# Kernel optimization log

Measured on AMD Instinct MI355X. Metric: run time of the kernel, lower is better.

## Reference

```python
import jax, jax.numpy as jnp
import numpy as np

NV = 117000
NE = 468000
EMB = 300
IN_DIM = 768
BATCH = 4096
HID = 500
NUM_LABELS = 2


def setup_inputs() -> dict:
    key = jax.random.key(0)
    ks = jax.random.split(key, 12)
    inp = {
        "input_tensor": jax.random.normal(ks[0], (BATCH, IN_DIM), dtype=jnp.float32),
        "node": jax.random.randint(ks[1], (BATCH,), 0, NV, dtype=jnp.int64),
        "edge_row": jax.random.randint(ks[2], (NE,), 0, NV, dtype=jnp.int32),
        "edge_col": jax.random.randint(ks[3], (NE,), 0, NV, dtype=jnp.int32),
        # learned parameters
        "H0": jax.random.normal(ks[4], (NV, EMB), dtype=jnp.float32) * 1.0,
        "W1": jax.random.normal(ks[5], (EMB, EMB), dtype=jnp.float32) * 0.01,
        "W2": jax.random.normal(ks[6], (EMB, EMB), dtype=jnp.float32) * 0.01,
        "Wa": jax.random.normal(ks[7], (IN_DIM + EMB, HID), dtype=jnp.float32) * 0.03,
        "ba": jnp.zeros((HID,), dtype=jnp.float32),
        "Wb": jax.random.normal(ks[8], (HID, HID), dtype=jnp.float32) * 0.04,
        "bb": jnp.zeros((HID,), dtype=jnp.float32),
        "Wc": jax.random.normal(ks[9], (HID, NUM_LABELS), dtype=jnp.float32) * 0.04,
        "bc": jnp.zeros((NUM_LABELS,), dtype=jnp.float32),
    }
    return inp


def reference(input_tensor, node, edge_row, edge_col, H0, W1, W2, Wa, ba, Wb, bb, Wc, bc):
    nV = H0.shape[0]
    # symmetric normalization D^{-1/2} A D^{-1/2} from edge list (duplicates sum, as in csr)
    deg = jax.ops.segment_sum(jnp.ones_like(edge_row, dtype=H0.dtype), edge_row, num_segments=nV)
    dinv = jnp.where(deg > 0, deg ** -0.5, 0.0)
    vals = dinv[edge_row] * dinv[edge_col]  # [nE]

    def spmm(X):  # LM @ X via gather + segment_sum
        return jax.ops.segment_sum(vals[:, None] * X[edge_col], edge_row, num_segments=nV)

    H1 = jax.nn.sigmoid(spmm(H0 @ W1))        # [nV, EMB]
    H2 = jax.nn.sigmoid(spmm(H1 @ W2))        # [nV, EMB]
    fc = jnp.concatenate([H2[node], input_tensor], axis=1)  # [B, EMB+IN_DIM]
    h = jax.nn.sigmoid(fc @ Wa + ba)
    h = jax.nn.sigmoid(h @ Wb + bb)
    return h @ Wc + bc                        # [B, NUM_LABELS]
```

## Files before the change

### kernel.cpp

```cpp
#include <hip/hip_runtime.h>
#include <hip/hip_bf16.h>

typedef __hip_bfloat16 bf16;

#define NVX 117000
#define NEX 468000
#define EMB 300
#define STR 320
#define IN_DIM 768
#define BATCH 4096
#define HID 500
#define FCK 1088
#define HPAD 512
#define NB 458
#define NEB 1829

#define CAP1 32768
#define CAP2 4096

#define PRE_W12 (384*STR)
#define PRE_WA  (HPAD*FCK)
#define PRE_WB  (HPAD*HPAD)
#define PRE_TOT (2*PRE_W12 + PRE_WA + PRE_WB)
#define PRE_BLK ((PRE_TOT+255)/256)

typedef __attribute__((ext_vector_type(8))) short frag8;
typedef __attribute__((ext_vector_type(4))) float f32x4;

__device__ __forceinline__ float sigmoidf_(float x){ return 1.0f/(1.0f + __expf(-x)); }
__device__ __forceinline__ float bfs2f(short s){
  return __uint_as_float(((unsigned int)(unsigned short)s) << 16);
}
__device__ __forceinline__ short f2bfs(float f){
  bf16 b = __float2bfloat16(f);
  return *(short*)&b;
}

__device__ __forceinline__ void gload_lds16(const bf16* g, bf16* l){
  __builtin_amdgcn_global_load_lds((const __attribute__((address_space(1))) void*)g,
                                   (__attribute__((address_space(3))) void*)l, 16, 0, 0);
}


__global__ __launch_bounds__(256) void k_setup(const int* __restrict__ erow,
                                               const int* __restrict__ node,
                                               int* __restrict__ deg,
                                               int* __restrict__ flag2,
                                               const float* __restrict__ W1,
                                               const float* __restrict__ W2,
                                               const float* __restrict__ Wa,
                                               const float* __restrict__ Wb,
                                               bf16* __restrict__ Wt1,
                                               bf16* __restrict__ Wt2,
                                               bf16* __restrict__ Wat,
                                               bf16* __restrict__ Wbt){
  long i = (long)blockIdx.x*256 + threadIdx.x;
  if (i < NEX) atomicAdd(&deg[erow[i]], 1);
  if (i < BATCH) flag2[node[i]] = 1;

  if (i < 2*PRE_W12){
    const float* W = (i < PRE_W12) ? W1 : W2;
    bf16* o = (i < PRE_W12) ? Wt1 : Wt2;
    int j = (int)((i < PRE_W12) ? i : i - PRE_W12);
    int n = j / STR, k = j % STR;
    float v = (n < EMB && k < EMB) ? W[k*EMB + n] : 0.0f;
    o[j] = __float2bfloat16(v);
    return;
  }
  i -= 2*PRE_W12;
  if (i < PRE_WA){
    int n = (int)(i / FCK), k = (int)(i % FCK);
    float v = 0.0f;
    if (n < HID){
      if (k < EMB)        v = Wa[(size_t)k*HID + n];
      else if (k >= STR)  v = Wa[(size_t)(k-(STR-EMB))*HID + n];
    }
    Wat[i] = __float2bfloat16(v);
    return;
  }
  i -= PRE_WA;
  if (i < PRE_WB){
    int n = (int)(i / HPAD), k = (int)(i % HPAD);
    float v = (n < HID && k < HID) ? Wb[(size_t)k*HID + n] : 0.0f;
    Wbt[i] = __float2bfloat16(v);
  }
}


__global__ __launch_bounds__(256) void k_flag1ps(const int* __restrict__ erow,
                                                 const int* __restrict__ ecol,
                                                 const int* __restrict__ flag2,
                                                 const int* __restrict__ deg,
                                                 int* __restrict__ flag1,
                                                 float* __restrict__ dinv,
                                                 int* __restrict__ bsum){
  int t = threadIdx.x;
  long j = (long)blockIdx.x*256 + t;
  if (j < NEX && flag2[erow[j]]) flag1[ecol[j]] = 1;

  if (blockIdx.x < NB){
    __shared__ int s[256];
    int i = blockIdx.x*256 + t;
    int d = (i < NVX) ? deg[i] : 0;
    if (i < NVX) dinv[i] = d > 0 ? rsqrtf((float)d) : 0.0f;
    s[t] = d;
    __syncthreads();
    #pragma unroll
    for (int off=128; off; off>>=1){
      if (t < off) s[t] += s[t+off];
      __syncthreads();
    }
    if (t == 0) bsum[blockIdx.x] = s[0];
  }
}


__global__ __launch_bounds__(256) void k_writeptr2(const int* __restrict__ deg,
                                                   const int* __restrict__ bsum,
                                                   int* __restrict__ rowptr,
                                                   int* __restrict__ cursor){
  __shared__ int sb[256];
  __shared__ int s[256];
  int t = threadIdx.x;
  int b = blockIdx.x;
  int acc = 0;
  for (int j = t; j < b; j += 256) acc += bsum[j];
  sb[t] = acc;
  __syncthreads();
  #pragma unroll
  for (int off=128; off; off>>=1){
    if (t < off) sb[t] += sb[t+off];
    __syncthreads();
  }
  int boff = sb[0];

  int i = b*256 + t;
  int v = (i < NVX) ? deg[i] : 0;
  s[t] = v; __syncthreads();
  #pragma unroll
  for (int off=1; off<256; off<<=1){
    int u = (t>=off) ? s[t-off] : 0;
    __syncthreads();
    s[t] += u;
    __syncthreads();
  }
  if (i < NVX){
    int e = boff + s[t] - v;
    rowptr[i] = e;
    cursor[i] = e;
  }
  if (b == 0 && t == 0) rowptr[NVX] = NEX;
}


__global__ __launch_bounds__(256) void k_edgec(const int* __restrict__ erow,
                                               const int* __restrict__ ecol,
                                               const float* __restrict__ dinv,
                                               const int* __restrict__ flag1,
                                               const int* __restrict__ flag2,
                                               int* __restrict__ cursor,
                                               int* __restrict__ ccol,
                                               float* __restrict__ cval,
                                               int* __restrict__ L1, int* __restrict__ inv1,
                                               int* __restrict__ L2, int* __restrict__ inv2,
                                               int* __restrict__ counts){
  long j = (long)blockIdx.x*256 + threadIdx.x;
  if (j < NEX){
    int r = erow[j];
    if (flag1[r] | flag2[r]){
      int c = ecol[j];
      int p = atomicAdd(&cursor[r], 1);
      ccol[p] = c;
      cval[p] = dinv[r]*dinv[c];
    }
  }
  int v = (int)j;
  if (v < NVX){
    if (flag1[v]){ int idx = atomicAdd(&counts[0], 1); if (idx < CAP1){ L1[idx] = v; inv1[v] = idx; } }
    if (flag2[v]){ int idx = atomicAdd(&counts[1], 1); if (idx < CAP2){ L2[idx] = v; inv2[v] = idx; } }
  }
}


__global__ __launch_bounds__(256) void k_spmm1(const int* __restrict__ rowptr,
                                               const int* __restrict__ ccol,
                                               const float* __restrict__ cval,
                                               const float* __restrict__ H0,
                                               const int* __restrict__ L1,
                                               const int* __restrict__ counts,
                                               bf16* __restrict__ Gc1){
  int i = (int)((blockIdx.x*blockDim.x + threadIdx.x) >> 6);
  int lane = threadIdx.x & 63;
  if (lane >= 40) return;
  int n1 = counts[0]; if (n1 > CAP1) n1 = CAP1;
  int n1pad = (n1 + 127) & ~127;
  if (i >= n1pad) return;
  int c0 = lane*8;
  bool hv1 = (c0 + 3) < EMB;
  bool hv2 = (c0 + 7) < EMB;
  float acc[8] = {0.f,0.f,0.f,0.f,0.f,0.f,0.f,0.f};
  if (i < n1 && hv1){
    int v = L1[i];
    int e0 = rowptr[v], e1 = rowptr[v+1];
    int e = e0;
    for (; e + 1 < e1; e += 2){
      float va = cval[e], vb = cval[e+1];
      const float* xa = H0 + (size_t)ccol[e  ]*EMB + c0;
      const float* xb = H0 + (size_t)ccol[e+1]*EMB + c0;
      float4 a0 = *(const float4*)xa;
      float4 b0 = *(const float4*)xb;
      float4 a1 = hv2 ? *(const float4*)(xa+4) : make_float4(0,0,0,0);
      float4 b1 = hv2 ? *(const float4*)(xb+4) : make_float4(0,0,0,0);
      acc[0] += va*a0.x + vb*b0.x;  acc[1] += va*a0.y + vb*b0.y;
      acc[2] += va*a0.z + vb*b0.z;  acc[3] += va*a0.w + vb*b0.w;
      acc[4] += va*a1.x + vb*b1.x;  acc[5] += va*a1.y + vb*b1.y;
      acc[6] += va*a1.z + vb*b1.z;  acc[7] += va*a1.w + vb*b1.w;
    }
    if (e < e1){
      float va = cval[e];
      const float* xa = H0 + (size_t)ccol[e]*EMB + c0;
      float4 a0 = *(const float4*)xa;
      float4 a1 = hv2 ? *(const float4*)(xa+4) : make_float4(0,0,0,0);
      acc[0] += va*a0.x; acc[1] += va*a0.y; acc[2] += va*a0.z; acc[3] += va*a0.w;
      acc[4] += va*a1.x; acc[5] += va*a1.y; acc[6] += va*a1.z; acc[7] += va*a1.w;
    }
  }
  frag8 o;
  #pragma unroll
  for (int j=0;j<8;++j) o[j] = f2bfs(acc[j]);
  *(frag8*)(Gc1 + (size_t)i*STR + c0) = o;
}


__global__ __launch_bounds__(256) void k_spmm2(const int* __restrict__ rowptr,
                                               const int* __restrict__ ccol,
                                               const float* __restrict__ cval,
                                               const bf16* __restrict__ Hc1,
                                               const int* __restrict__ inv1,
                                               const int* __restrict__ L2,
                                               const int* __restrict__ counts,
                                               bf16* __restrict__ Gc2){
  int i = (int)((blockIdx.x*blockDim.x + threadIdx.x) >> 6);
  int lane = threadIdx.x & 63;
  if (lane >= 40) return;
  int n2 = counts[1]; if (n2 > CAP2) n2 = CAP2;
  int n2pad = (n2 + 127) & ~127;
  if (i >= n2pad) return;
  float acc[8] = {0.f,0.f,0.f,0.f,0.f,0.f,0.f,0.f};
  if (i < n2){
    int v = L2[i];
    int e0 = rowptr[v], e1 = rowptr[v+1];
    int e = e0;
    for (; e + 1 < e1; e += 2){
      float va = cval[e], vb = cval[e+1];
      frag8 xa = *(const frag8*)(Hc1 + (size_t)inv1[ccol[e  ]]*STR + lane*8);
      frag8 xb = *(const frag8*)(Hc1 + (size_t)inv1[ccol[e+1]]*STR + lane*8);
      #pragma unroll
      for (int j=0;j<8;++j) acc[j] += va*bfs2f(xa[j]) + vb*bfs2f(xb[j]);
    }
    if (e < e1){
      float va = cval[e];
      frag8 xa = *(const frag8*)(Hc1 + (size_t)inv1[ccol[e]]*STR + lane*8);
      #pragma unroll
      for (int j=0;j<8;++j) acc[j] += va*bfs2f(xa[j]);
    }
  }
  frag8 o;
  #pragma unroll
  for (int j=0;j<8;++j) o[j] = f2bfs(acc[j]);
  *(frag8*)(Gc2 + (size_t)i*STR + lane*8) = o;
}


__global__ __launch_bounds__(256) void k_gemm_node(const bf16* __restrict__ A,
                                                   const bf16* __restrict__ Wt,
                                                   bf16* __restrict__ C,
                                                   const int* __restrict__ counts, int which){
  const int row0 = blockIdx.y * 128;
  if (row0 >= counts[which]) return;
  __shared__ bf16 As[128*32];
  __shared__ bf16 Bs[128*32];
  const int tid  = threadIdx.x;
  const int wv   = tid >> 6;
  const int lane = tid & 63;
  const int n0   = blockIdx.x * 128;
  const int wm = wv & 1, wn = wv >> 1;
  const int srow = lane >> 2;
  const int schk = lane & 3;
  const int fr = lane & 15, fq = lane >> 4;

  f32x4 acc[4][4];
  #pragma unroll
  for (int i=0;i<4;++i)
    #pragma unroll
    for (int j=0;j<4;++j) acc[i][j] = (f32x4)(0.0f);

  for (int k0 = 0; k0 < STR; k0 += 32){
    const bf16* ag = A + (size_t)(row0 + wv*16 + srow)*STR + k0 + schk*8;
    gload_lds16(ag,           As + wv*512 + lane*8);
    gload_lds16(ag + 64*STR,  As + 2048 + wv*512 + lane*8);
    const bf16* bg = Wt + (size_t)(n0 + wv*16 + srow)*STR + k0 + schk*8;
    gload_lds16(bg,           Bs + wv*512 + lane*8);
    gload_lds16(bg + 64*STR,  Bs + 2048 + wv*512 + lane*8);
    __syncthreads();
    frag8 a[4], b[4];
    #pragma unroll
    for (int mi=0;mi<4;++mi)
      a[mi] = *(const frag8*)(As + (wm*64 + mi*16 + fr)*32 + fq*8);
    #pragma unroll
    for (int ni=0;ni<4;++ni)
      b[ni] = *(const frag8*)(Bs + (wn*64 + ni*16 + fr)*32 + fq*8);
    #pragma unroll
    for (int mi=0;mi<4;++mi)
      #pragma unroll
      for (int ni=0;ni<4;++ni)
        acc[mi][ni] = __builtin_amdgcn_mfma_f32_16x16x32_bf16(a[mi], b[ni], acc[mi][ni], 0, 0, 0);
    __syncthreads();
  }

  #pragma unroll
  for (int mi=0;mi<4;++mi){
    int row = row0 + wm*64 + mi*16 + fq*4;
    #pragma unroll
    for (int ni=0;ni<4;++ni){
      int col = n0 + wn*64 + ni*16 + fr;
      if (col < STR){
        bf16* cp = C + (size_t)row*STR + col;
        #pragma unroll
        for (int r=0;r<4;++r){
          float v = (col < EMB) ? sigmoidf_(acc[mi][ni][r]) : 0.0f;
          cp[(size_t)r*STR] = __float2bfloat16(v);
        }
      }
    }
  }
}


__global__ __launch_bounds__(256) void k_fc1g(const bf16* __restrict__ Hc2,
                                              const int* __restrict__ node,
                                              const int* __restrict__ inv2,
                                              const float* __restrict__ input,
                                              const bf16* __restrict__ Wat,
                                              const float* __restrict__ ba,
                                              bf16* __restrict__ h1){
  __shared__ bf16 As[128*32];
  __shared__ bf16 Bs[128*32];
  const int tid  = threadIdx.x;
  const int wv   = tid >> 6;
  const int lane = tid & 63;
  const int row0 = blockIdx.y * 128;
  const int n0   = blockIdx.x * 128;
  const int wm = wv & 1, wn = wv >> 1;
  const int srow = lane >> 2;
  const int schk = lane & 3;
  const int fr = lane & 15, fq = lane >> 4;

  const int nlo = inv2[node[row0 + wv*16 + srow]];
  const int nhi = inv2[node[row0 + 64 + wv*16 + srow]];

  f32x4 acc[4][4];
  #pragma unroll
  for (int i=0;i<4;++i)
    #pragma unroll
    for (int j=0;j<4;++j) acc[i][j] = (f32x4)(0.0f);

  for (int k0 = 0; k0 < FCK; k0 += 32){
    if (k0 < STR){
      gload_lds16(Hc2 + (size_t)nlo*STR + k0 + schk*8, As + wv*512 + lane*8);
      gload_lds16(Hc2 + (size_t)nhi*STR + k0 + schk*8, As + 2048 + wv*512 + lane*8);
    } else {
      int c = k0 - STR + schk*8;
      int m0 = wv*16 + srow;
      float4 u0 = *(const float4*)(input + (size_t)(row0+m0)*IN_DIM + c);
      float4 u1 = *(const float4*)(input + (size_t)(row0+m0)*IN_DIM + c + 4);
      frag8 t0;
      t0[0]=f2bfs(u0.x); t0[1]=f2bfs(u0.y); t0[2]=f2bfs(u0.z); t0[3]=f2bfs(u0.w);
      t0[4]=f2bfs(u1.x); t0[5]=f2bfs(u1.y); t0[6]=f2bfs(u1.z); t0[7]=f2bfs(u1.w);
      *(frag8*)(As + m0*32 + schk*8) = t0;
      int m1 = 64 + wv*16 + srow;
      float4 u2 = *(const float4*)(input + (size_t)(row0+m1)*IN_DIM + c);
      float4 u3 = *(const float4*)(input + (size_t)(row0+m1)*IN_DIM + c + 4);
      frag8 t1;
      t1[0]=f2bfs(u2.x); t1[1]=f2bfs(u2.y); t1[2]=f2bfs(u2.z); t1[3]=f2bfs(u2.w);
      t1[4]=f2bfs(u3.x); t1[5]=f2bfs(u3.y); t1[6]=f2bfs(u3.z); t1[7]=f2bfs(u3.w);
      *(frag8*)(As + m1*32 + schk*8) = t1;
    }
    gload_lds16(Wat + (size_t)(n0 + wv*16 + srow)*FCK + k0 + schk*8, Bs + wv*512 + lane*8);
    gload_lds16(Wat + (size_t)(n0 + 64 + wv*16 + srow)*FCK + k0 + schk*8, Bs + 2048 + wv*512 + lane*8);
    __syncthreads();
    frag8 a[4], b[4];
    #pragma unroll
    for (int mi=0;mi<4;++mi)
      a[mi] = *(const frag8*)(As + (wm*64 + mi*16 + fr)*32 + fq*8);
    #pragma unroll
    for (int ni=0;ni<4;++ni)
      b[ni] = *(const frag8*)(Bs + (wn*64 + ni*16 + fr)*32 + fq*8);
    #pragma unroll
    for (int mi=0;mi<4;++mi)
      #pragma unroll
      for (int ni=0;ni<4;++ni)
        acc[mi][ni] = __builtin_amdgcn_mfma_f32_16x16x32_bf16(a[mi], b[ni], acc[mi][ni], 0, 0, 0);
    __syncthreads();
  }

  #pragma unroll
  for (int mi=0;mi<4;++mi){
    int row = row0 + wm*64 + mi*16 + fq*4;
    #pragma unroll
    for (int ni=0;ni<4;++ni){
      int col = n0 + wn*64 + ni*16 + fr;
      float bv = (col < HID) ? ba[col] : 0.0f;
      bf16* cp = h1 + (size_t)row*HPAD + col;
      #pragma unroll
      for (int r=0;r<4;++r)
        cp[(size_t)r*HPAD] = __float2bfloat16(sigmoidf_(acc[mi][ni][r] + bv));
    }
  }
}


__global__ __launch_bounds__(256) void k_fc2o(const bf16* __restrict__ A,
                                              const bf16* __restrict__ B,
                                              const float* __restrict__ bb,
                                              const float* __restrict__ Wc,
                                              const float* __restrict__ bc,
                                              float* __restrict__ out){
  __shared__ bf16 As[128*32];
  __shared__ bf16 Bs[128*32];
  const int tid  = threadIdx.x;
  const int wv   = tid >> 6;
  const int lane = tid & 63;
  const int row0 = blockIdx.y * 128;
  const int n0   = blockIdx.x * 128;
  const int wm = wv & 1, wn = wv >> 1;
  const int srow = lane >> 2;
  const int schk = lane & 3;
  const int fr = lane & 15, fq = lane >> 4;

  f32x4 acc[4][4];
  #pragma unroll
  for (int i=0;i<4;++i)
    #pragma unroll
    for (int j=0;j<4;++j) acc[i][j] = (f32x4)(0.0f);

  for (int k0 = 0; k0 < HPAD; k0 += 32){
    const bf16* ag = A + (size_t)(row0 + wv*16 + srow)*HPAD + k0 + schk*8;
    gload_lds16(ag,            As + wv*512 + lane*8);
    gload_lds16(ag + 64*HPAD,  As + 2048 + wv*512 + lane*8);
    const bf16* bg = B + (size_t)(n0 + wv*16 + srow)*HPAD + k0 + schk*8;
    gload_lds16(bg,            Bs + wv*512 + lane*8);
    gload_lds16(bg + 64*HPAD,  Bs + 2048 + wv*512 + lane*8);
    __syncthreads();
    frag8 a[4], b[4];
    #pragma unroll
    for (int mi=0;mi<4;++mi)
      a[mi] = *(const frag8*)(As + (wm*64 + mi*16 + fr)*32 + fq*8);
    #pragma unroll
    for (int ni=0;ni<4;++ni)
      b[ni] = *(const frag8*)(Bs + (wn*64 + ni*16 + fr)*32 + fq*8);
    #pragma unroll
    for (int mi=0;mi<4;++mi)
      #pragma unroll
      for (int ni=0;ni<4;++ni)
        acc[mi][ni] = __builtin_amdgcn_mfma_f32_16x16x32_bf16(a[mi], b[ni], acc[mi][ni], 0, 0, 0);
    __syncthreads();
  }

  #pragma unroll
  for (int mi=0;mi<4;++mi){
    #pragma unroll
    for (int r=0;r<4;++r){
      int row = row0 + wm*64 + mi*16 + fq*4 + r;
      float s0 = 0.0f, s1 = 0.0f;
      #pragma unroll
      for (int ni=0;ni<4;++ni){
        int col = n0 + wn*64 + ni*16 + fr;
        if (col < HID){
          float v = sigmoidf_(acc[mi][ni][r] + bb[col]);
          s0 += v * Wc[col*2+0];
          s1 += v * Wc[col*2+1];
        }
      }
      #pragma unroll
      for (int off=1; off<16; off<<=1){
        s0 += __shfl_xor(s0, off);
        s1 += __shfl_xor(s1, off);
      }
      if (fr == 0){
        if (n0 == 0 && wn == 0){ s0 += bc[0]; s1 += bc[1]; }
        atomicAdd(out + (size_t)row*2 + 0, s0);
        atomicAdd(out + (size_t)row*2 + 1, s1);
      }
    }
  }
}


extern "C" void kernel_launch(void* const* d_in, const int* in_sizes, int n_in,
                              void* d_out, int out_size, void* d_ws, size_t ws_size,
                              hipStream_t stream){
  const float* input = (const float*)d_in[0];
  const int*   node  = (const int*)d_in[1];
  const int*   erow  = (const int*)d_in[2];
  const int*   ecol  = (const int*)d_in[3];
  const float* H0    = (const float*)d_in[4];
  const float* W1    = (const float*)d_in[5];
  const float* W2    = (const float*)d_in[6];
  const float* Wa    = (const float*)d_in[7];
  const float* ba    = (const float*)d_in[8];
  const float* Wb    = (const float*)d_in[9];
  const float* bb    = (const float*)d_in[10];
  const float* Wc    = (const float*)d_in[11];
  const float* bc    = (const float*)d_in[12];

  char* p = (char*)d_ws;
  auto alloc = [&](size_t bytes)->char*{ char* r = p; p += (bytes + 255) & ~(size_t)255; return r; };
  char* z0     = p;
  int*   deg    = (int*)  alloc((size_t)NVX*4);
  int*   flag1  = (int*)  alloc((size_t)NVX*4);
  int*   flag2  = (int*)  alloc((size_t)NVX*4);
  int*   counts = (int*)  alloc(256);
  size_t zlen   = (size_t)(p - z0);
  float* dinv   = (float*)alloc((size_t)NVX*4);
  int*   rowptr = (int*)  alloc((size_t)(NVX+1)*4);
  int*   cursor = (int*)  alloc((size_t)NVX*4);
  int*   bsum   = (int*)  alloc((size_t)NB*4);
  int*   ccol   = (int*)  alloc((size_t)NEX*4);
  float* cval   = (float*)alloc((size_t)NEX*4);
  int*   L1     = (int*)  alloc((size_t)CAP1*4);
  int*   inv1   = (int*)  alloc((size_t)NVX*4);
  int*   L2     = (int*)  alloc((size_t)CAP2*4);
  int*   inv2   = (int*)  alloc((size_t)NVX*4);
  bf16*  Gc1    = (bf16*) alloc((size_t)CAP1*STR*2);
  bf16*  Hc1    = (bf16*) alloc((size_t)CAP1*STR*2);
  bf16*  Gc2    = (bf16*) alloc((size_t)CAP2*STR*2);
  bf16*  Hc2    = (bf16*) alloc((size_t)CAP2*STR*2);
  bf16*  Wt1    = (bf16*) alloc((size_t)384*STR*2);
  bf16*  Wt2    = (bf16*) alloc((size_t)384*STR*2);
  bf16*  Wat    = (bf16*) alloc((size_t)HPAD*FCK*2);
  bf16*  Wbt    = (bf16*) alloc((size_t)HPAD*HPAD*2);
  bf16*  h1     = (bf16*) alloc((size_t)BATCH*HPAD*2);

  hipMemsetAsync(z0, 0, zlen, stream);
  hipMemsetAsync(d_out, 0, (size_t)out_size*4, stream);

  k_setup<<<PRE_BLK, 256, 0, stream>>>(erow, node, deg, flag2, W1, W2, Wa, Wb, Wt1, Wt2, Wat, Wbt);
  k_flag1ps<<<NEB, 256, 0, stream>>>(erow, ecol, flag2, deg, flag1, dinv, bsum);
  k_writeptr2<<<NB, 256, 0, stream>>>(deg, bsum, rowptr, cursor);
  k_edgec<<<NEB, 256, 0, stream>>>(erow, ecol, dinv, flag1, flag2, cursor, ccol, cval,
                                   L1, inv1, L2, inv2, counts);

  k_spmm1    <<<CAP1/4, 256, 0, stream>>>(rowptr, ccol, cval, H0, L1, counts, Gc1);
  k_gemm_node<<<dim3(3, CAP1/128), 256, 0, stream>>>(Gc1, Wt1, Hc1, counts, 0);
  k_spmm2    <<<CAP2/4, 256, 0, stream>>>(rowptr, ccol, cval, Hc1, inv1, L2, counts, Gc2);
  k_gemm_node<<<dim3(3, CAP2/128), 256, 0, stream>>>(Gc2, Wt2, Hc2, counts, 1);

  k_fc1g<<<dim3(HPAD/128, BATCH/128), 256, 0, stream>>>(Hc2, node, inv2, input, Wat, ba, h1);
  k_fc2o<<<dim3(HPAD/128, BATCH/128), 256, 0, stream>>>(h1, Wbt, bb, Wc, bc, (float*)d_out);
}
```

Before: 407.7 us.

## Merge preprocessing and layer-2 stages into cooperative kernels with grid syncs

Replaces two memsets and four preprocessing kernels with a single cooperative kernel that zeroes its own buffers and separates phases with grid-wide syncs. It also fuses the second sparse aggregation and its node GEMM into one cooperative kernel, and unrolls the first SpMM edge loop by four. The aim is to remove kernel launch gaps and memset overhead. In exchange, each phase runs on a smaller persistent grid with grid-stride loops, and grid syncs add their own cost.

```diff
diff --git a/kernel.cpp b/kernel.cpp
--- a/kernel.cpp
+++ b/kernel.cpp
@@ -1,5 +1,8 @@
 #include <hip/hip_runtime.h>
 #include <hip/hip_bf16.h>
+#include <hip/hip_cooperative_groups.h>
+
+namespace cg = cooperative_groups;
 
 typedef __hip_bfloat16 bf16;
 
@@ -13,7 +16,6 @@
 #define FCK 1088
 #define HPAD 512
 #define NB 458
-#define NEB 1829
 
 #define CAP1 32768
 #define CAP2 4096
@@ -22,7 +24,6 @@
 #define PRE_WA  (HPAD*FCK)
 #define PRE_WB  (HPAD*HPAD)
 #define PRE_TOT (2*PRE_W12 + PRE_WA + PRE_WB)
-#define PRE_BLK ((PRE_TOT+255)/256)
 
 typedef __attribute__((ext_vector_type(8))) short frag8;
 typedef __attribute__((ext_vector_type(4))) float f32x4;
@@ -42,130 +43,117 @@
 }
 
 
-__global__ __launch_bounds__(256) void k_setup(const int* __restrict__ erow,
-                                               const int* __restrict__ node,
-                                               int* __restrict__ deg,
-                                               int* __restrict__ flag2,
-                                               const float* __restrict__ W1,
-                                               const float* __restrict__ W2,
-                                               const float* __restrict__ Wa,
-                                               const float* __restrict__ Wb,
-                                               bf16* __restrict__ Wt1,
-                                               bf16* __restrict__ Wt2,
-                                               bf16* __restrict__ Wat,
-                                               bf16* __restrict__ Wbt){
-  long i = (long)blockIdx.x*256 + threadIdx.x;
-  if (i < NEX) atomicAdd(&deg[erow[i]], 1);
-  if (i < BATCH) flag2[node[i]] = 1;
-
-  if (i < 2*PRE_W12){
-    const float* W = (i < PRE_W12) ? W1 : W2;
-    bf16* o = (i < PRE_W12) ? Wt1 : Wt2;
-    int j = (int)((i < PRE_W12) ? i : i - PRE_W12);
-    int n = j / STR, k = j % STR;
-    float v = (n < EMB && k < EMB) ? W[k*EMB + n] : 0.0f;
-    o[j] = __float2bfloat16(v);
-    return;
-  }
-  i -= 2*PRE_W12;
-  if (i < PRE_WA){
-    int n = (int)(i / FCK), k = (int)(i % FCK);
-    float v = 0.0f;
-    if (n < HID){
-      if (k < EMB)        v = Wa[(size_t)k*HID + n];
-      else if (k >= STR)  v = Wa[(size_t)(k-(STR-EMB))*HID + n];
-    }
-    Wat[i] = __float2bfloat16(v);
-    return;
-  }
-  i -= PRE_WA;
-  if (i < PRE_WB){
-    int n = (int)(i / HPAD), k = (int)(i % HPAD);
-    float v = (n < HID && k < HID) ? Wb[(size_t)k*HID + n] : 0.0f;
-    Wbt[i] = __float2bfloat16(v);
-  }
-}
-
-
-__global__ __launch_bounds__(256) void k_flag1ps(const int* __restrict__ erow,
-                                                 const int* __restrict__ ecol,
-                                                 const int* __restrict__ flag2,
-                                                 const int* __restrict__ deg,
-                                                 int* __restrict__ flag1,
-                                                 float* __restrict__ dinv,
-                                                 int* __restrict__ bsum){
-  int t = threadIdx.x;
-  long j = (long)blockIdx.x*256 + t;
-  if (j < NEX && flag2[erow[j]]) flag1[ecol[j]] = 1;
-
-  if (blockIdx.x < NB){
-    __shared__ int s[256];
-    int i = blockIdx.x*256 + t;
-    int d = (i < NVX) ? deg[i] : 0;
-    if (i < NVX) dinv[i] = d > 0 ? rsqrtf((float)d) : 0.0f;
-    s[t] = d;
-    __syncthreads();
-    #pragma unroll
-    for (int off=128; off; off>>=1){
-      if (t < off) s[t] += s[t+off];
+__global__ __launch_bounds__(256) void k_pre(
+    const int* __restrict__ erow, const int* __restrict__ ecol,
+    const int* __restrict__ node,
+    const float* __restrict__ W1, const float* __restrict__ W2,
+    const float* __restrict__ Wa, const float* __restrict__ Wb,
+    int* __restrict__ deg, int* __restrict__ flag1, int* __restrict__ flag2,
+    int* __restrict__ counts, float* __restrict__ dinv, int* __restrict__ bsum,
+    int* __restrict__ rowptr, int* __restrict__ cursor,
+    int* __restrict__ ccol, float* __restrict__ cval,
+    int* __restrict__ L1, int* __restrict__ inv1,
+    int* __restrict__ L2, int* __restrict__ inv2,
+    bf16* __restrict__ Wt1, bf16* __restrict__ Wt2,
+    bf16* __restrict__ Wat, bf16* __restrict__ Wbt,
+    float* __restrict__ outp)
+{
+  const int t   = threadIdx.x;
+  const int tid = blockIdx.x*256 + t;
+  const int T   = gridDim.x*256;
+
+  for (int i = tid; i < NVX; i += T){ deg[i]=0; flag1[i]=0; flag2[i]=0; }
+  if (tid < 64) counts[tid] = 0;
+  for (int i = tid; i < BATCH*2; i += T) outp[i] = 0.0f;
+  cg::this_grid().sync();
+
+  for (int i = tid; i < NEX; i += T) atomicAdd(&deg[erow[i]], 1);
+  if (tid < BATCH) flag2[node[tid]] = 1;
+  for (long w = tid; w < PRE_TOT; w += T){
+    long i = w;
+    if (i < 2*PRE_W12){
+      const float* W = (i < PRE_W12) ? W1 : W2;
+      bf16* o = (i < PRE_W12) ? Wt1 : Wt2;
+      int j = (int)((i < PRE_W12) ? i : i - PRE_W12);
+      int n = j / STR, k = j % STR;
+      float v = (n < EMB && k < EMB) ? W[k*EMB + n] : 0.0f;
+      o[j] = __float2bfloat16(v);
+    } else {
+      i -= 2*PRE_W12;
+      if (i < PRE_WA){
+        int n = (int)(i / FCK), k = (int)(i % FCK);
+        float v = 0.0f;
+        if (n < HID){
+          if (k < EMB)        v = Wa[(size_t)k*HID + n];
+          else if (k >= STR)  v = Wa[(size_t)(k-(STR-EMB))*HID + n];
+        }
+        Wat[i] = __float2bfloat16(v);
+      } else {
+        i -= PRE_WA;
+        int n = (int)(i / HPAD), k = (int)(i % HPAD);
+        float v = (n < HID && k < HID) ? Wb[(size_t)k*HID + n] : 0.0f;
+        Wbt[i] = __float2bfloat16(v);
+      }
+    }
+  }
+  cg::this_grid().sync();
+
+  for (int i = tid; i < NEX; i += T) if (flag2[erow[i]]) flag1[ecol[i]] = 1;
+  {
+    __shared__ int s2[256];
+    for (int c = blockIdx.x; c < NB; c += gridDim.x){
+      int i = c*256 + t;
+      int d = (i < NVX) ? deg[i] : 0;
+      if (i < NVX) dinv[i] = d > 0 ? rsqrtf((float)d) : 0.0f;
+      s2[t] = d;
       __syncthreads();
-    }
-    if (t == 0) bsum[blockIdx.x] = s[0];
-  }
-}
-
-
-__global__ __launch_bounds__(256) void k_writeptr2(const int* __restrict__ deg,
-                                                   const int* __restrict__ bsum,
-                                                   int* __restrict__ rowptr,
-                                                   int* __restrict__ cursor){
-  __shared__ int sb[256];
-  __shared__ int s[256];
-  int t = threadIdx.x;
-  int b = blockIdx.x;
-  int acc = 0;
-  for (int j = t; j < b; j += 256) acc += bsum[j];
-  sb[t] = acc;
-  __syncthreads();
-  #pragma unroll
-  for (int off=128; off; off>>=1){
-    if (t < off) sb[t] += sb[t+off];
-    __syncthreads();
-  }
-  int boff = sb[0];
-
-  int i = b*256 + t;
-  int v = (i < NVX) ? deg[i] : 0;
-  s[t] = v; __syncthreads();
-  #pragma unroll
-  for (int off=1; off<256; off<<=1){
-    int u = (t>=off) ? s[t-off] : 0;
-    __syncthreads();
-    s[t] += u;
-    __syncthreads();
-  }
-  if (i < NVX){
-    int e = boff + s[t] - v;
-    rowptr[i] = e;
-    cursor[i] = e;
-  }
-  if (b == 0 && t == 0) rowptr[NVX] = NEX;
-}
-
-
-__global__ __launch_bounds__(256) void k_edgec(const int* __restrict__ erow,
-                                               const int* __restrict__ ecol,
-                                               const float* __restrict__ dinv,
-                                               const int* __restrict__ flag1,
-                                               const int* __restrict__ flag2,
-                                               int* __restrict__ cursor,
-                                               int* __restrict__ ccol,
-                                               float* __restrict__ cval,
-                                               int* __restrict__ L1, int* __restrict__ inv1,
-                                               int* __restrict__ L2, int* __restrict__ inv2,
-                                               int* __restrict__ counts){
-  long j = (long)blockIdx.x*256 + threadIdx.x;
-  if (j < NEX){
+      #pragma unroll
+      for (int off=128; off; off>>=1){
+        if (t < off) s2[t] += s2[t+off];
+        __syncthreads();
+      }
+      if (t == 0) bsum[c] = s2[0];
+      __syncthreads();
+    }
+  }
+  cg::this_grid().sync();
+
+  {
+    __shared__ int sb[256];
+    __shared__ int s3[256];
+    for (int c = blockIdx.x; c < NB; c += gridDim.x){
+      int acc = 0;
+      for (int j = t; j < c; j += 256) acc += bsum[j];
+      sb[t] = acc;
+      __syncthreads();
+      #pragma unroll
+      for (int off=128; off; off>>=1){
+        if (t < off) sb[t] += sb[t+off];
+        __syncthreads();
+      }
+      int boff = sb[0];
+      int i = c*256 + t;
+      int v = (i < NVX) ? deg[i] : 0;
+      s3[t] = v; __syncthreads();
+      #pragma unroll
+      for (int off=1; off<256; off<<=1){
+        int u = (t>=off) ? s3[t-off] : 0;
+        __syncthreads();
+        s3[t] += u;
+        __syncthreads();
+      }
+      if (i < NVX){
+        int e = boff + s3[t] - v;
+        rowptr[i] = e;
+        cursor[i] = e;
+      }
+      __syncthreads();
+    }
+    if (tid == 0) rowptr[NVX] = NEX;
+  }
+  cg::this_grid().sync();
+
+  for (int j = tid; j < NEX; j += T){
     int r = erow[j];
     if (flag1[r] | flag2[r]){
       int c = ecol[j];
@@ -174,8 +162,7 @@
       cval[p] = dinv[r]*dinv[c];
     }
   }
-  int v = (int)j;
-  if (v < NVX){
+  for (int v = tid; v < NVX; v += T){
     if (flag1[v]){ int idx = atomicAdd(&counts[0], 1); if (idx < CAP1){ L1[idx] = v; inv1[v] = idx; } }
     if (flag2[v]){ int idx = atomicAdd(&counts[1], 1); if (idx < CAP2){ L2[idx] = v; inv2[v] = idx; } }
   }
@@ -203,6 +190,30 @@
     int v = L1[i];
     int e0 = rowptr[v], e1 = rowptr[v+1];
     int e = e0;
+    for (; e + 3 < e1; e += 4){
+      float w0 = cval[e], w1 = cval[e+1], w2 = cval[e+2], w3 = cval[e+3];
+      const float* p0 = H0 + (size_t)ccol[e  ]*EMB + c0;
+      const float* p1 = H0 + (size_t)ccol[e+1]*EMB + c0;
+      const float* p2 = H0 + (size_t)ccol[e+2]*EMB + c0;
+      const float* p3 = H0 + (size_t)ccol[e+3]*EMB + c0;
+      float4 A0 = *(const float4*)p0, B0 = *(const float4*)p1;
+      float4 C0 = *(const float4*)p2, D0 = *(const float4*)p3;
+      float4 A1, B1, C1, D1;
+      if (hv2){
+        A1 = *(const float4*)(p0+4); B1 = *(const float4*)(p1+4);
+        C1 = *(const float4*)(p2+4); D1 = *(const float4*)(p3+4);
+      } else {
+        A1 = B1 = C1 = D1 = make_float4(0,0,0,0);
+      }
+      acc[0] += w0*A0.x + w1*B0.x + w2*C0.x + w3*D0.x;
+      acc[1] += w0*A0.y + w1*B0.y + w2*C0.y + w3*D0.y;
+      acc[2] += w0*A0.z + w1*B0.z + w2*C0.z + w3*D0.z;
+      acc[3] += w0*A0.w + w1*B0.w + w2*C0.w + w3*D0.w;
+      acc[4] += w0*A1.x + w1*B1.x + w2*C1.x + w3*D1.x;
+      acc[5] += w0*A1.y + w1*B1.y + w2*C1.y + w3*D1.y;
+      acc[6] += w0*A1.z + w1*B1.z + w2*C1.z + w3*D1.z;
+      acc[7] += w0*A1.w + w1*B1.w + w2*C1.w + w3*D1.w;
+    }
     for (; e + 1 < e1; e += 2){
       float va = cval[e], vb = cval[e+1];
       const float* xa = H0 + (size_t)ccol[e  ]*EMB + c0;
@@ -232,58 +243,14 @@
 }
 
 
-__global__ __launch_bounds__(256) void k_spmm2(const int* __restrict__ rowptr,
-                                               const int* __restrict__ ccol,
-                                               const float* __restrict__ cval,
-                                               const bf16* __restrict__ Hc1,
-                                               const int* __restrict__ inv1,
-                                               const int* __restrict__ L2,
-                                               const int* __restrict__ counts,
-                                               bf16* __restrict__ Gc2){
-  int i = (int)((blockIdx.x*blockDim.x + threadIdx.x) >> 6);
-  int lane = threadIdx.x & 63;
-  if (lane >= 40) return;
-  int n2 = counts[1]; if (n2 > CAP2) n2 = CAP2;
-  int n2pad = (n2 + 127) & ~127;
-  if (i >= n2pad) return;
-  float acc[8] = {0.f,0.f,0.f,0.f,0.f,0.f,0.f,0.f};
-  if (i < n2){
-    int v = L2[i];
-    int e0 = rowptr[v], e1 = rowptr[v+1];
-    int e = e0;
-    for (; e + 1 < e1; e += 2){
-      float va = cval[e], vb = cval[e+1];
-      frag8 xa = *(const frag8*)(Hc1 + (size_t)inv1[ccol[e  ]]*STR + lane*8);
-      frag8 xb = *(const frag8*)(Hc1 + (size_t)inv1[ccol[e+1]]*STR + lane*8);
-      #pragma unroll
-      for (int j=0;j<8;++j) acc[j] += va*bfs2f(xa[j]) + vb*bfs2f(xb[j]);
-    }
-    if (e < e1){
-      float va = cval[e];
-      frag8 xa = *(const frag8*)(Hc1 + (size_t)inv1[ccol[e]]*STR + lane*8);
-      #pragma unroll
-      for (int j=0;j<8;++j) acc[j] += va*bfs2f(xa[j]);
-    }
-  }
-  frag8 o;
-  #pragma unroll
-  for (int j=0;j<8;++j) o[j] = f2bfs(acc[j]);
-  *(frag8*)(Gc2 + (size_t)i*STR + lane*8) = o;
-}
-
-
-__global__ __launch_bounds__(256) void k_gemm_node(const bf16* __restrict__ A,
-                                                   const bf16* __restrict__ Wt,
-                                                   bf16* __restrict__ C,
-                                                   const int* __restrict__ counts, int which){
-  const int row0 = blockIdx.y * 128;
-  if (row0 >= counts[which]) return;
-  __shared__ bf16 As[128*32];
-  __shared__ bf16 Bs[128*32];
+__device__ __forceinline__ void gemm_tile_body(const bf16* __restrict__ A,
+                                               const bf16* __restrict__ Wt,
+                                               bf16* __restrict__ C,
+                                               int row0, int n0,
+                                               bf16* As, bf16* Bs){
   const int tid  = threadIdx.x;
   const int wv   = tid >> 6;
   const int lane = tid & 63;
-  const int n0   = blockIdx.x * 128;
   const int wm = wv & 1, wn = wv >> 1;
   const int srow = lane >> 2;
   const int schk = lane & 3;
@@ -332,6 +299,78 @@
           cp[(size_t)r*STR] = __float2bfloat16(v);
         }
       }
+    }
+  }
+}
+
+__global__ __launch_bounds__(256) void k_gemm_node(const bf16* __restrict__ A,
+                                                   const bf16* __restrict__ Wt,
+                                                   bf16* __restrict__ C,
+                                                   const int* __restrict__ counts, int which){
+  const int row0 = blockIdx.y * 128;
+  if (row0 >= counts[which]) return;
+  __shared__ bf16 As[128*32];
+  __shared__ bf16 Bs[128*32];
+  gemm_tile_body(A, Wt, C, row0, blockIdx.x * 128, As, Bs);
+}
+
+
+__global__ __launch_bounds__(256) void k_l2(const int* __restrict__ rowptr,
+                                            const int* __restrict__ ccol,
+                                            const float* __restrict__ cval,
+                                            const bf16* __restrict__ Hc1,
+                                            const int* __restrict__ inv1,
+                                            const int* __restrict__ L2,
+                                            const int* __restrict__ counts,
+                                            bf16* __restrict__ Gc2,
+                                            const bf16* __restrict__ Wt2,
+                                            bf16* __restrict__ Hc2){
+  __shared__ bf16 As[128*32];
+  __shared__ bf16 Bs[128*32];
+
+  {
+    const int lane = threadIdx.x & 63;
+    const int gw = (int)((blockIdx.x*256 + threadIdx.x) >> 6);
+    const int NW = gridDim.x * 4;
+    int n2 = counts[1]; if (n2 > CAP2) n2 = CAP2;
+    int n2pad = (n2 + 127) & ~127;
+    if (lane < 40){
+      for (int i = gw; i < n2pad; i += NW){
+        float acc[8] = {0.f,0.f,0.f,0.f,0.f,0.f,0.f,0.f};
+        if (i < n2){
+          int v = L2[i];
+          int e0 = rowptr[v], e1 = rowptr[v+1];
+          int e = e0;
+          for (; e + 1 < e1; e += 2){
+            float va = cval[e], vb = cval[e+1];
+            frag8 xa = *(const frag8*)(Hc1 + (size_t)inv1[ccol[e  ]]*STR + lane*8);
+            frag8 xb = *(const frag8*)(Hc1 + (size_t)inv1[ccol[e+1]]*STR + lane*8);
+            #pragma unroll
+            for (int j=0;j<8;++j) acc[j] += va*bfs2f(xa[j]) + vb*bfs2f(xb[j]);
+          }
+          if (e < e1){
+            float va = cval[e];
+            frag8 xa = *(const frag8*)(Hc1 + (size_t)inv1[ccol[e]]*STR + lane*8);
+            #pragma unroll
+            for (int j=0;j<8;++j) acc[j] += va*bfs2f(xa[j]);
+          }
+        }
+        frag8 o;
+        #pragma unroll
+        for (int j=0;j<8;++j) o[j] = f2bfs(acc[j]);
+        *(frag8*)(Gc2 + (size_t)i*STR + lane*8) = o;
+      }
+    }
+  }
+  cg::this_grid().sync();
+
+  {
+    const int b = blockIdx.x;
+    if (b < 96){
+      const int n0   = (b % 3) * 128;
+      const int row0 = (b / 3) * 128;
+      if (row0 < counts[1])
+        gemm_tile_body(Gc2, Wt2, Hc2, row0, n0, As, Bs);
     }
   }
 }
@@ -513,15 +552,14 @@
   const float* bb    = (const float*)d_in[10];
   const float* Wc    = (const float*)d_in[11];
   const float* bc    = (const float*)d_in[12];
+  float* outp = (float*)d_out;
 
   char* p = (char*)d_ws;
   auto alloc = [&](size_t bytes)->char*{ char* r = p; p += (bytes + 255) & ~(size_t)255; return r; };
-  char* z0     = p;
   int*   deg    = (int*)  alloc((size_t)NVX*4);
   int*   flag1  = (int*)  alloc((size_t)NVX*4);
   int*   flag2  = (int*)  alloc((size_t)NVX*4);
   int*   counts = (int*)  alloc(256);
-  size_t zlen   = (size_t)(p - z0);
   float* dinv   = (float*)alloc((size_t)NVX*4);
   int*   rowptr = (int*)  alloc((size_t)(NVX+1)*4);
   int*   cursor = (int*)  alloc((size_t)NVX*4);
@@ -542,20 +580,48 @@
   bf16*  Wbt    = (bf16*) alloc((size_t)HPAD*HPAD*2);
   bf16*  h1     = (bf16*) alloc((size_t)BATCH*HPAD*2);
 
-  hipMemsetAsync(z0, 0, zlen, stream);
-  hipMemsetAsync(d_out, 0, (size_t)out_size*4, stream);
-
-  k_setup<<<PRE_BLK, 256, 0, stream>>>(erow, node, deg, flag2, W1, W2, Wa, Wb, Wt1, Wt2, Wat, Wbt);
-  k_flag1ps<<<NEB, 256, 0, stream>>>(erow, ecol, flag2, deg, flag1, dinv, bsum);
-  k_writeptr2<<<NB, 256, 0, stream>>>(deg, bsum, rowptr, cursor);
-  k_edgec<<<NEB, 256, 0, stream>>>(erow, ecol, dinv, flag1, flag2, cursor, ccol, cval,
-                                   L1, inv1, L2, inv2, counts);
-
-  k_spmm1    <<<CAP1/4, 256, 0, stream>>>(rowptr, ccol, cval, H0, L1, counts, Gc1);
+  static int gb_pre = 0, gb_l2 = 0;
+  if (gb_pre == 0){
+    int o1 = 0, o2 = 0;
+    hipOccupancyMaxActiveBlocksPerMultiprocessor(&o1, k_pre, 256, 0);
+    hipOccupancyMaxActiveBlocksPerMultiprocessor(&o2, k_l2, 256, 0);
+    if (o1 < 1) o1 = 1;
+    if (o2 < 1) o2 = 1;
+    int g1 = o1 * 256; if (g1 > 1024) g1 = 1024;
+    int g2 = o2 * 256; if (g2 > 512)  g2 = 512;
+    gb_l2  = g2;
+    gb_pre = g1;
+  }
+
+  {
+    void* kargs[] = {
+      (void*)&erow, (void*)&ecol, (void*)&node,
+      (void*)&W1, (void*)&W2, (void*)&Wa, (void*)&Wb,
+      (void*)&deg, (void*)&flag1, (void*)&flag2,
+      (void*)&counts, (void*)&dinv, (void*)&bsum,
+      (void*)&rowptr, (void*)&cursor,
+      (void*)&ccol, (void*)&cval,
+      (void*)&L1, (void*)&inv1, (void*)&L2, (void*)&inv2,
+      (void*)&Wt1, (void*)&Wt2, (void*)&Wat, (void*)&Wbt,
+      (void*)&outp
+    };
+    hipLaunchCooperativeKernel(reinterpret_cast<const void*>(&k_pre),
+                               dim3(gb_pre), dim3(256), kargs, 0, stream);
+  }
+
+  k_spmm1<<<CAP1/4, 256, 0, stream>>>(rowptr, ccol, cval, H0, L1, counts, Gc1);
   k_gemm_node<<<dim3(3, CAP1/128), 256, 0, stream>>>(Gc1, Wt1, Hc1, counts, 0);
-  k_spmm2    <<<CAP2/4, 256, 0, stream>>>(rowptr, ccol, cval, Hc1, inv1, L2, counts, Gc2);
-  k_gemm_node<<<dim3(3, CAP2/128), 256, 0, stream>>>(Gc2, Wt2, Hc2, counts, 1);
+
+  {
+    void* kargs[] = {
+      (void*)&rowptr, (void*)&ccol, (void*)&cval,
+      (void*)&Hc1, (void*)&inv1, (void*)&L2, (void*)&counts,
+      (void*)&Gc2, (void*)&Wt2, (void*)&Hc2
+    };
+    hipLaunchCooperativeKernel(reinterpret_cast<const void*>(&k_l2),
+                               dim3(gb_l2), dim3(256), kargs, 0, stream);
+  }
 
   k_fc1g<<<dim3(HPAD/128, BATCH/128), 256, 0, stream>>>(Hc2, node, inv2, input, Wat, ba, h1);
-  k_fc2o<<<dim3(HPAD/128, BATCH/128), 256, 0, stream>>>(h1, Wbt, bb, Wc, bc, (float*)d_out);
-}
+  k_fc2o<<<dim3(HPAD/128, BATCH/128), 256, 0, stream>>>(h1, Wbt, bb, Wc, bc, outp);
+}
```

Result: slower. 863.5 us (+111.8%).
